# Kernel optimization log

Hardware: AMD Instinct MI355X
Metric: run time of the kernel (lower is better)

## Reference

```python
import jax, jax.numpy as jnp
import numpy as np

N = 10000
E = 320000
DIN = 256
HID = 64
HEADS = 4
LAT = 32
NEG_SLOPE = 0.2


def _layer_params(key, din, heads, out_c):
    ks = jax.random.split(key, 6)
    s_in = 1.0 / np.sqrt(din)
    return dict(
        Wl=jax.random.normal(ks[0], (din, heads * out_c), jnp.float32) * s_in,
        bl=jnp.zeros((heads * out_c,), jnp.float32),
        Wr=jax.random.normal(ks[1], (din, heads * out_c), jnp.float32) * s_in,
        br=jnp.zeros((heads * out_c,), jnp.float32),
        att=jax.random.normal(ks[2], (heads, out_c), jnp.float32) * (1.0 / np.sqrt(out_c)),
        bo=jnp.zeros((heads * out_c,), jnp.float32),
    )


def setup_inputs() -> dict:
    key = jax.random.key(0)
    ks = jax.random.split(key, 8)
    inp = {
        "x": jax.random.normal(ks[0], (N, DIN), jnp.float32),
        "edge_index": jax.random.randint(ks[1], (2, E), 0, N, jnp.int64 if jax.config.jax_enable_x64 else jnp.int32),
        "eps": jax.random.normal(ks[2], (N, LAT), jnp.float32),
    }
    p0 = _layer_params(ks[3], DIN, HEADS, HID)
    p1 = _layer_params(ks[4], HID * HEADS, HEADS, HID)
    pmu = _layer_params(ks[5], HID * HEADS, 1, LAT)
    plv = _layer_params(ks[6], HID * HEADS, 1, LAT)
    for tag, p in (("l0", p0), ("l1", p1), ("mu", pmu), ("lv", plv)):
        for k, v in p.items():
            inp[f"{k}_{tag}"] = v
    return inp


def _gatv2(h, src, dst, Wl, bl, Wr, br, att, bo, heads, out_c, concat):
    # GATv2: e_ij = att . LeakyReLU(lin_l(x_j) + lin_r(x_i)), softmax over j for each i,
    # out_i = sum_j alpha_ij * lin_l(x_j). src = j (source), dst = i (target).
    xl = (h @ Wl + bl).reshape(-1, heads, out_c)  # [N,H,C]
    xr = (h @ Wr + br).reshape(-1, heads, out_c)
    e = jax.nn.leaky_relu(xl[src] + xr[dst], NEG_SLOPE)  # [E,H,C]
    score = jnp.einsum('ehc,hc->eh', e, att)             # [E,H]
    smax = jax.ops.segment_max(score, dst, num_segments=N)
    ex = jnp.exp(score - smax[dst])
    denom = jax.ops.segment_sum(ex, dst, num_segments=N)
    alpha = ex / (denom[dst] + 1e-16)                    # [E,H]
    out = jax.ops.segment_sum(alpha[:, :, None] * xl[src], dst, num_segments=N)  # [N,H,C]
    out = out.reshape(N, heads * out_c) if concat else out.mean(axis=1)
    return out + bo


def reference(x, edge_index, eps,
              Wl_l0, bl_l0, Wr_l0, br_l0, att_l0, bo_l0,
              Wl_l1, bl_l1, Wr_l1, br_l1, att_l1, bo_l1,
              Wl_mu, bl_mu, Wr_mu, br_mu, att_mu, bo_mu,
              Wl_lv, bl_lv, Wr_lv, br_lv, att_lv, bo_lv):
    loop = jnp.arange(N, dtype=edge_index.dtype)
    src = jnp.concatenate([edge_index[0], loop])  # add self-loops (PyG default)
    dst = jnp.concatenate([edge_index[1], loop])
    h = jax.nn.elu(_gatv2(x, src, dst, Wl_l0, bl_l0, Wr_l0, br_l0, att_l0, bo_l0, HEADS, HID, True))
    h = jax.nn.elu(_gatv2(h, src, dst, Wl_l1, bl_l1, Wr_l1, br_l1, att_l1, bo_l1, HEADS, HID, True))
    mu = _gatv2(h, src, dst, Wl_mu, bl_mu, Wr_mu, br_mu, att_mu, bo_mu, 1, LAT, False)
    log_var = _gatv2(h, src, dst, Wl_lv, bl_lv, Wr_lv, br_lv, att_lv, bo_lv, 1, LAT, False)
    z = mu + eps * jnp.exp(0.5 * log_var)  # reparameterize (training mode)
    adj_recon = z @ z.T                    # [N,N] dense decode
    return (adj_recon, mu, log_var)
```

## Files before the change

kernel.cpp:

```cpp
#include <hip/hip_runtime.h>
#include <hip/hip_bf16.h>
#include <math.h>

constexpr int Nn  = 10000;
constexpr int Ed  = 320000;
constexpr int DIN = 256;
constexpr float NEG = 0.2f;

constexpr size_t OFF_XL  = 0;
constexpr size_t OFF_XR  = 2560000;
constexpr size_t OFF_H   = 5120000;
constexpr size_t OFF_XSL = 7680000;
constexpr size_t OFF_XSR = 8320000;
constexpr size_t OFF_WLC = 8960000;
constexpr size_t OFF_WRC = 8976384;
constexpr size_t OFF_BLC = 8992768;
constexpr size_t OFF_BRC = 8992832;
constexpr size_t OFF_ATT = 8992896;
constexpr size_t OFF_BOC = 8992960;
constexpr size_t OFF_INT = 9000000;
constexpr int I_DEG = 0;
constexpr int I_ROW = 16384;
constexpr int I_CUR = 32768;
constexpr int I_CSR = 49152;
static_assert(OFF_INT + (I_CSR + Ed + Nn + 4) < 100000000, "scratch fits in adj region");

__device__ __forceinline__ unsigned short f2bf(float x) {
    unsigned int u = __float_as_uint(x);
    unsigned int r = (u + 0x7FFFu + ((u >> 16) & 1u)) >> 16;
    return (unsigned short)r;
}
__device__ __forceinline__ float bf2f(unsigned short b) {
    return __uint_as_float(((unsigned int)b) << 16);
}

typedef short bf16x8 __attribute__((ext_vector_type(8)));
typedef float f32x4  __attribute__((ext_vector_type(4)));

__global__ void k_init_deg(int* deg, int n) {
    int i = blockIdx.x * blockDim.x + threadIdx.x;
    if (i < n) deg[i] = 1;
}

__global__ void k_count(const int* __restrict__ dst, int* deg, int e) {
    int i = blockIdx.x * blockDim.x + threadIdx.x;
    if (i < e) atomicAdd(&deg[dst[i]], 1);
}

__global__ void k_scan(const int* __restrict__ deg, int* row_ptr, int* cursor, int n) {
    __shared__ int sums[256];
    int t = threadIdx.x;
    int chunk = (n + 255) / 256;
    int start = t * chunk, end = min(start + chunk, n);
    int s = 0;
    for (int i = start; i < end; ++i) s += deg[i];
    sums[t] = s;
    __syncthreads();
    for (int off = 1; off < 256; off <<= 1) {
        int v = (t >= off) ? sums[t - off] : 0;
        __syncthreads();
        sums[t] += v;
        __syncthreads();
    }
    int run = sums[t] - s;
    for (int i = start; i < end; ++i) { row_ptr[i] = run; cursor[i] = run; run += deg[i]; }
    if (t == 255) row_ptr[n] = sums[255];
}

__global__ void k_scatter(const int* __restrict__ src, const int* __restrict__ dst,
                          int* cursor, int* csr, int e, int n) {
    int i = blockIdx.x * blockDim.x + threadIdx.x;
    if (i < e) {
        int d = dst[i];
        int pos = atomicAdd(&cursor[d], 1);
        csr[pos] = src[i];
    } else if (i < e + n) {
        int v = i - e;
        int pos = atomicAdd(&cursor[v], 1);
        csr[pos] = v;
    }
}

template <int NC>
__global__ __launch_bounds__(256) void k_gemm2(const float* __restrict__ A,
                                               const float* __restrict__ WL,
                                               const float* __restrict__ biasL,
                                               unsigned short* __restrict__ outL,
                                               const float* __restrict__ WR,
                                               const float* __restrict__ biasR,
                                               float* __restrict__ outR,
                                               int M) {
    constexpr int K = 256;
    __shared__ float As[32][68];
    __shared__ float WsL[32][64];
    __shared__ float WsR[32][64];
    int tid = threadIdx.x;
    int tx = tid & 15, ty = tid >> 4;
    int m0 = blockIdx.x * 64, n0 = blockIdx.y * 64;
    float accL[4][4] = {}, accR[4][4] = {};
    int am = tid >> 2, akb = (tid & 3) * 8;
    int wk = tid >> 3, wnb = (tid & 7) * 8;
    const bool arow_ok = (m0 + am) < M;
    const float* Aptr  = A  + (size_t)(m0 + am) * K + akb;
    const float* WLptr = WL + (size_t)wk * NC + n0 + wnb;
    const float* WRptr = WR + (size_t)wk * NC + n0 + wnb;

    for (int k0 = 0; k0 < K; k0 += 32) {
        float4 a0 = {0, 0, 0, 0}, a1 = {0, 0, 0, 0};
        if (arow_ok) {
            a0 = *(const float4*)(Aptr + k0);
            a1 = *(const float4*)(Aptr + k0 + 4);
        }
        float4 wl0 = *(const float4*)(WLptr + (size_t)k0 * NC);
        float4 wl1 = *(const float4*)(WLptr + (size_t)k0 * NC + 4);
        float4 wr0 = *(const float4*)(WRptr + (size_t)k0 * NC);
        float4 wr1 = *(const float4*)(WRptr + (size_t)k0 * NC + 4);
        __syncthreads();
        As[akb + 0][am] = a0.x; As[akb + 1][am] = a0.y; As[akb + 2][am] = a0.z; As[akb + 3][am] = a0.w;
        As[akb + 4][am] = a1.x; As[akb + 5][am] = a1.y; As[akb + 6][am] = a1.z; As[akb + 7][am] = a1.w;
        *(float4*)&WsL[wk][wnb]     = wl0;
        *(float4*)&WsL[wk][wnb + 4] = wl1;
        *(float4*)&WsR[wk][wnb]     = wr0;
        *(float4*)&WsR[wk][wnb + 4] = wr1;
        __syncthreads();
        #pragma unroll
        for (int k = 0; k < 32; ++k) {
            float4 a  = *(const float4*)&As[k][ty * 4];
            float4 bl = *(const float4*)&WsL[k][tx * 4];
            float4 br = *(const float4*)&WsR[k][tx * 4];
            float av[4]  = {a.x, a.y, a.z, a.w};
            float blv[4] = {bl.x, bl.y, bl.z, bl.w};
            float brv[4] = {br.x, br.y, br.z, br.w};
            #pragma unroll
            for (int i2 = 0; i2 < 4; ++i2)
                #pragma unroll
                for (int j2 = 0; j2 < 4; ++j2) {
                    accL[i2][j2] = fmaf(av[i2], blv[j2], accL[i2][j2]);
                    accR[i2][j2] = fmaf(av[i2], brv[j2], accR[i2][j2]);
                }
        }
    }
    #pragma unroll
    for (int i2 = 0; i2 < 4; ++i2) {
        int row = m0 + ty * 4 + i2;
        if (row < M) {
            int col = n0 + tx * 4;
            ushort4 s;
            s.x = f2bf(accL[i2][0] + biasL[col + 0]);
            s.y = f2bf(accL[i2][1] + biasL[col + 1]);
            s.z = f2bf(accL[i2][2] + biasL[col + 2]);
            s.w = f2bf(accL[i2][3] + biasL[col + 3]);
            *(ushort4*)&outL[(size_t)row * NC + col] = s;
            float4 o;
            o.x = accR[i2][0] + biasR[col + 0];
            o.y = accR[i2][1] + biasR[col + 1];
            o.z = accR[i2][2] + biasR[col + 2];
            o.w = accR[i2][3] + biasR[col + 3];
            *(float4*)&outR[(size_t)row * NC + col] = o;
        }
    }
}

__device__ __forceinline__ float lrelu(float x) { return x > 0.f ? x : NEG * x; }

template <bool DO_ELU>
__global__ __launch_bounds__(256) void k_gat4(const unsigned short* __restrict__ xl,
                                              const float* __restrict__ xr,
                                              const float* __restrict__ att,
                                              const float* __restrict__ bo,
                                              const int* __restrict__ row_ptr,
                                              const int* __restrict__ csr,
                                              float* __restrict__ out, int n) {
    int lane = threadIdx.x & 63;
    int node = (blockIdx.x * blockDim.x + threadIdx.x) >> 6;
    if (node >= n) return;
    int f = lane * 4;
    float4 xrr  = *(const float4*)&xr[(size_t)node * 256 + f];
    float4 attr = *(const float4*)&att[f];
    float m = -INFINITY, d = 0.f;
    float4 acc = {0.f, 0.f, 0.f, 0.f};

    int e0 = row_ptr[node], e1 = row_ptr[node + 1];
    int e = e0;
    for (; e + 1 < e1; e += 2) {
        int ja = csr[e], jb = csr[e + 1];
        ushort4 ua = *(const ushort4*)&xl[(size_t)ja * 256 + f];
        ushort4 ub = *(const ushort4*)&xl[(size_t)jb * 256 + f];
        float4 va = {bf2f(ua.x), bf2f(ua.y), bf2f(ua.z), bf2f(ua.w)};
        float4 vb = {bf2f(ub.x), bf2f(ub.y), bf2f(ub.z), bf2f(ub.w)};
        float ta = attr.x * lrelu(va.x + xrr.x) + attr.y * lrelu(va.y + xrr.y)
                 + attr.z * lrelu(va.z + xrr.z) + attr.w * lrelu(va.w + xrr.w);
        float tb = attr.x * lrelu(vb.x + xrr.x) + attr.y * lrelu(vb.y + xrr.y)
                 + attr.z * lrelu(vb.z + xrr.z) + attr.w * lrelu(vb.w + xrr.w);
        #pragma unroll
        for (int mask = 1; mask <= 8; mask <<= 1) {
            ta += __shfl_xor(ta, mask, 64);
            tb += __shfl_xor(tb, mask, 64);
        }
        float mn = fmaxf(m, fmaxf(ta, tb));
        float sc = __expf(m - mn);
        float pa = __expf(ta - mn), pb = __expf(tb - mn);
        d = d * sc + pa + pb;
        acc.x = acc.x * sc + pa * va.x + pb * vb.x;
        acc.y = acc.y * sc + pa * va.y + pb * vb.y;
        acc.z = acc.z * sc + pa * va.z + pb * vb.z;
        acc.w = acc.w * sc + pa * va.w + pb * vb.w;
        m = mn;
    }
    if (e < e1) {
        int j = csr[e];
        ushort4 u = *(const ushort4*)&xl[(size_t)j * 256 + f];
        float4 v = {bf2f(u.x), bf2f(u.y), bf2f(u.z), bf2f(u.w)};
        float t = attr.x * lrelu(v.x + xrr.x) + attr.y * lrelu(v.y + xrr.y)
                + attr.z * lrelu(v.z + xrr.z) + attr.w * lrelu(v.w + xrr.w);
        #pragma unroll
        for (int mask = 1; mask <= 8; mask <<= 1) t += __shfl_xor(t, mask, 64);
        float mn = fmaxf(m, t);
        float sc = __expf(m - mn), p = __expf(t - mn);
        d = d * sc + p;
        acc.x = acc.x * sc + p * v.x;
        acc.y = acc.y * sc + p * v.y;
        acc.z = acc.z * sc + p * v.z;
        acc.w = acc.w * sc + p * v.w;
        m = mn;
    }
    float inv = 1.f / (d + 1e-16f);
    float4 bo4 = *(const float4*)&bo[f];
    float4 o;
    o.x = acc.x * inv + bo4.x;
    o.y = acc.y * inv + bo4.y;
    o.z = acc.z * inv + bo4.z;
    o.w = acc.w * inv + bo4.w;
    if (DO_ELU) {
        o.x = o.x > 0.f ? o.x : expm1f(o.x);
        o.y = o.y > 0.f ? o.y : expm1f(o.y);
        o.z = o.z > 0.f ? o.z : expm1f(o.z);
        o.w = o.w > 0.f ? o.w : expm1f(o.w);
    }
    *(float4*)&out[(size_t)node * 256 + f] = o;
}

__global__ __launch_bounds__(256) void k_gatz(const unsigned short* __restrict__ xl,
                                              const float* __restrict__ xr,
                                              const float* __restrict__ att,
                                              const float* __restrict__ bo,
                                              const int* __restrict__ row_ptr,
                                              const int* __restrict__ csr,
                                              const float* __restrict__ eps,
                                              float* __restrict__ out0,
                                              float* __restrict__ out1,
                                              unsigned short* __restrict__ zhi,
                                              unsigned short* __restrict__ zlo, int n) {
    constexpr int C = 32;
    int lane = threadIdx.x & 63;
    int node = (blockIdx.x * blockDim.x + threadIdx.x) >> 6;
    if (node >= n) return;

    float xrr  = xr[(size_t)node * 64 + lane];
    float attr = att[lane];
    float m = -INFINITY, d = 0.f, acc = 0.f;

    int e0 = row_ptr[node], e1 = row_ptr[node + 1];
    for (int e = e0; e < e1; ++e) {
        int j = csr[e];
        float v = bf2f(xl[(size_t)j * 64 + lane]);
        float t = v + xrr;
        t = (t > 0.f) ? t : NEG * t;
        t *= attr;
        #pragma unroll
        for (int mask = C / 2; mask >= 1; mask >>= 1)
            t += __shfl_xor(t, mask, 64);
        if (t > m) {
            float sc = __expf(m - t);
            d *= sc; acc *= sc; m = t;
        }
        float p = __expf(t - m);
        d += p;
        acc = fmaf(p, v, acc);
    }
    float o = acc / (d + 1e-16f) + bo[lane];
    int c = lane & 31;
    float* op = (lane < 32) ? out0 : out1;
    op[(size_t)node * C + c] = o;
    float lvv = __shfl(o, lane + 32, 64);
    if (zhi != nullptr && lane < 32) {
        float zc = o + eps[(size_t)node * 32 + lane] * __expf(0.5f * lvv);
        unsigned short h = f2bf(zc);
        zhi[(size_t)node * 32 + lane] = h;
        zlo[(size_t)node * 32 + lane] = f2bf(zc - bf2f(h));
    }
}

__global__ void k_cat(const float* __restrict__ Wlmu, const float* __restrict__ Wllv,
                      const float* __restrict__ Wrmu, const float* __restrict__ Wrlv,
                      const float* __restrict__ blmu, const float* __restrict__ bllv,
                      const float* __restrict__ brmu, const float* __restrict__ brlv,
                      const float* __restrict__ attmu, const float* __restrict__ attlv,
                      const float* __restrict__ bomu, const float* __restrict__ bolv,
                      float* WLC, float* WRC, float* BLC, float* BRC, float* ATTC, float* BOC) {
    int i = blockIdx.x * blockDim.x + threadIdx.x;
    if (i < 256 * 64) {
        int k = i >> 6, c = i & 63;
        WLC[i] = (c < 32) ? Wlmu[k * 32 + c] : Wllv[k * 32 + c - 32];
        WRC[i] = (c < 32) ? Wrmu[k * 32 + c] : Wrlv[k * 32 + c - 32];
    }
    if (i < 64) {
        BLC[i]  = (i < 32) ? blmu[i]  : bllv[i - 32];
        BRC[i]  = (i < 32) ? brmu[i]  : brlv[i - 32];
        ATTC[i] = (i < 32) ? attmu[i] : attlv[i - 32];
        BOC[i]  = (i < 32) ? bomu[i]  : bolv[i - 32];
    }
}

constexpr int JTM = 25;

__global__ __launch_bounds__(256) void k_adjm(const unsigned short* __restrict__ zhi,
                                              const unsigned short* __restrict__ zlo,
                                              float* __restrict__ adj, int n) {
    int wave  = threadIdx.x >> 6;
    int l     = threadIdx.x & 63;
    int strip = blockIdx.y * 4 + wave;
    if (strip * 16 >= n) return;
    int i0   = strip * 16;
    int arow = i0 + (l & 15);
    int koff = (l >> 4) * 8;
    bf16x8 a_hi = *(const bf16x8*)(zhi + (size_t)arow * 32 + koff);
    bf16x8 a_lo = *(const bf16x8*)(zlo + (size_t)arow * 32 + koff);
    int crow = i0 + (l >> 4) * 4;

    for (int t = 0; t < JTM; ++t) {
        int j0   = (blockIdx.x * JTM + t) * 16;
        int brow = j0 + (l & 15);
        bf16x8 b_hi = *(const bf16x8*)(zhi + (size_t)brow * 32 + koff);
        bf16x8 b_lo = *(const bf16x8*)(zlo + (size_t)brow * 32 + koff);
        f32x4 acc = {0.f, 0.f, 0.f, 0.f};
        acc = __builtin_amdgcn_mfma_f32_16x16x32_bf16(a_hi, b_hi, acc, 0, 0, 0);
        acc = __builtin_amdgcn_mfma_f32_16x16x32_bf16(a_hi, b_lo, acc, 0, 0, 0);
        acc = __builtin_amdgcn_mfma_f32_16x16x32_bf16(a_lo, b_hi, acc, 0, 0, 0);
        size_t base = (size_t)crow * n + j0 + (l & 15);
        adj[base]                 = acc[0];
        adj[base + (size_t)n]     = acc[1];
        adj[base + (size_t)n * 2] = acc[2];
        adj[base + (size_t)n * 3] = acc[3];
    }
}

constexpr int JT = 8;
__global__ __launch_bounds__(256) void k_adj_fb(const float* __restrict__ mu,
                                                const float* __restrict__ lv,
                                                const float* __restrict__ eps,
                                                float* __restrict__ adj, int n) {
    __shared__ float Zi[32][68];
    __shared__ float Zj[32][68];
    int tid = threadIdx.x;
    int tx = tid & 15, ty = tid >> 4;
    int i0 = blockIdx.y * 64;
    int r = tid >> 2, kq = (tid & 3) * 8;

    auto load8 = [&](int row, float4& a, float4& b) {
        a = make_float4(0.f, 0.f, 0.f, 0.f);
        b = make_float4(0.f, 0.f, 0.f, 0.f);
        if (row < n) {
            float4 m0 = *(const float4*)&mu[row * 32 + kq];
            float4 l0 = *(const float4*)&lv[row * 32 + kq];
            float4 e0 = *(const float4*)&eps[row * 32 + kq];
            float4 m1 = *(const float4*)&mu[row * 32 + kq + 4];
            float4 l1 = *(const float4*)&lv[row * 32 + kq + 4];
            float4 e1 = *(const float4*)&eps[row * 32 + kq + 4];
            a.x = m0.x + e0.x * __expf(0.5f * l0.x);
            a.y = m0.y + e0.y * __expf(0.5f * l0.y);
            a.z = m0.z + e0.z * __expf(0.5f * l0.z);
            a.w = m0.w + e0.w * __expf(0.5f * l0.w);
            b.x = m1.x + e1.x * __expf(0.5f * l1.x);
            b.y = m1.y + e1.y * __expf(0.5f * l1.y);
            b.z = m1.z + e1.z * __expf(0.5f * l1.z);
            b.w = m1.w + e1.w * __expf(0.5f * l1.w);
        }
    };

    {
        float4 a, b;
        load8(i0 + r, a, b);
        Zi[kq + 0][r] = a.x; Zi[kq + 1][r] = a.y; Zi[kq + 2][r] = a.z; Zi[kq + 3][r] = a.w;
        Zi[kq + 4][r] = b.x; Zi[kq + 5][r] = b.y; Zi[kq + 6][r] = b.z; Zi[kq + 7][r] = b.w;
    }
    __syncthreads();
    float4 af[32];
    #pragma unroll
    for (int k = 0; k < 32; ++k) af[k] = *(const float4*)&Zi[k][ty * 4];

    for (int jt = 0; jt < JT; ++jt) {
        int j0 = (blockIdx.x * JT + jt) * 64;
        if (j0 >= n) break;
        {
            float4 a, b;
            load8(j0 + r, a, b);
            __syncthreads();
            Zj[kq + 0][r] = a.x; Zj[kq + 1][r] = a.y; Zj[kq + 2][r] = a.z; Zj[kq + 3][r] = a.w;
            Zj[kq + 4][r] = b.x; Zj[kq + 5][r] = b.y; Zj[kq + 6][r] = b.z; Zj[kq + 7][r] = b.w;
            __syncthreads();
        }
        float acc[4][4] = {};
        #pragma unroll
        for (int k = 0; k < 32; ++k) {
            float4 b = *(const float4*)&Zj[k][tx * 4];
            float av[4] = {af[k].x, af[k].y, af[k].z, af[k].w};
            float bv[4] = {b.x, b.y, b.z, b.w};
            #pragma unroll
            for (int i2 = 0; i2 < 4; ++i2)
                #pragma unroll
                for (int j2 = 0; j2 < 4; ++j2)
                    acc[i2][j2] = fmaf(av[i2], bv[j2], acc[i2][j2]);
        }
        int col = j0 + tx * 4;
        if (col < n) {
            #pragma unroll
            for (int i2 = 0; i2 < 4; ++i2) {
                int row = i0 + ty * 4 + i2;
                if (row < n) {
                    float4 o = {acc[i2][0], acc[i2][1], acc[i2][2], acc[i2][3]};
                    *(float4*)&adj[(size_t)row * n + col] = o;
                }
            }
        }
    }
}

extern "C" void kernel_launch(void* const* d_in, const int* in_sizes, int n_in,
                              void* d_out, int out_size, void* d_ws, size_t ws_size,
                              hipStream_t stream) {
    const float* x      = (const float*)d_in[0];
    const int*   edges  = (const int*)d_in[1];
    const float* eps    = (const float*)d_in[2];
    const float* Wl0 = (const float*)d_in[3];
    const float* bl0 = (const float*)d_in[4];
    const float* Wr0 = (const float*)d_in[5];
    const float* br0 = (const float*)d_in[6];
    const float* at0 = (const float*)d_in[7];
    const float* bo0 = (const float*)d_in[8];
    const float* Wl1 = (const float*)d_in[9];
    const float* bl1 = (const float*)d_in[10];
    const float* Wr1 = (const float*)d_in[11];
    const float* br1 = (const float*)d_in[12];
    const float* at1 = (const float*)d_in[13];
    const float* bo1 = (const float*)d_in[14];
    const float* Wlmu = (const float*)d_in[15];
    const float* blmu = (const float*)d_in[16];
    const float* Wrmu = (const float*)d_in[17];
    const float* brmu = (const float*)d_in[18];
    const float* atmu = (const float*)d_in[19];
    const float* bomu = (const float*)d_in[20];
    const float* Wllv = (const float*)d_in[21];
    const float* bllv = (const float*)d_in[22];
    const float* Wrlv = (const float*)d_in[23];
    const float* brlv = (const float*)d_in[24];
    const float* atlv = (const float*)d_in[25];
    const float* bolv = (const float*)d_in[26];

    float* base   = (float*)d_out;
    float* adj    = base;
    float* mu_out = base + (size_t)Nn * Nn;
    float* lv_out = mu_out + (size_t)Nn * 32;

    unsigned short* XLB  = (unsigned short*)(base + OFF_XL);
    float* XR  = base + OFF_XR;
    float* H   = base + OFF_H;
    unsigned short* XSLB = (unsigned short*)(base + OFF_XSL);
    float* XSR = base + OFF_XSR;
    float* WLC = base + OFF_WLC;
    float* WRC = base + OFF_WRC;
    float* BLC = base + OFF_BLC;
    float* BRC = base + OFF_BRC;
    float* ATT = base + OFF_ATT;
    float* BOC = base + OFF_BOC;
    int* ib  = (int*)(base + OFF_INT);
    int* deg = ib + I_DEG;
    int* row = ib + I_ROW;
    int* cur = ib + I_CUR;
    int* csr = ib + I_CSR;
    const int* srcp = edges;
    const int* dstp = edges + Ed;

    size_t need = (size_t)Nn * 32 * 2 * sizeof(unsigned short);
    unsigned short* zhi = (ws_size >= need) ? (unsigned short*)d_ws : nullptr;
    unsigned short* zlo = zhi ? zhi + (size_t)Nn * 32 : nullptr;

    k_init_deg<<<(Nn + 255) / 256, 256, 0, stream>>>(deg, Nn);
    k_count<<<(Ed + 255) / 256, 256, 0, stream>>>(dstp, deg, Ed);
    k_scan<<<1, 256, 0, stream>>>(deg, row, cur, Nn);
    k_scatter<<<(Ed + Nn + 255) / 256, 256, 0, stream>>>(srcp, dstp, cur, csr, Ed, Nn);

    dim3 g4(157, 4), g1(157, 1);
    k_gemm2<256><<<g4, 256, 0, stream>>>(x, Wl0, bl0, XLB, Wr0, br0, XR, Nn);
    k_gat4<true><<<2500, 256, 0, stream>>>(XLB, XR, at0, bo0, row, csr, H, Nn);
    k_gemm2<256><<<g4, 256, 0, stream>>>(H, Wl1, bl1, XLB, Wr1, br1, XR, Nn);
    k_gat4<true><<<2500, 256, 0, stream>>>(XLB, XR, at1, bo1, row, csr, H, Nn);
    k_cat<<<64, 256, 0, stream>>>(Wlmu, Wllv, Wrmu, Wrlv, blmu, bllv, brmu, brlv,
                                  atmu, atlv, bomu, bolv, WLC, WRC, BLC, BRC, ATT, BOC);
    k_gemm2<64><<<g1, 256, 0, stream>>>(H, WLC, BLC, XSLB, WRC, BRC, XSR, Nn);
    k_gatz<<<2500, 256, 0, stream>>>(XSLB, XSR, ATT, BOC, row, csr, eps,
                                     mu_out, lv_out, zhi, zlo, Nn);

    if (zhi) {
        dim3 ga(25, 157);
        k_adjm<<<ga, 256, 0, stream>>>(zhi, zlo, adj, Nn);
    } else {
        dim3 ga(20, 157);
        k_adj_fb<<<ga, 256, 0, stream>>>(mu_out, lv_out, eps, adj, Nn);
    }
}
```

Baseline: 408.5 us.

## Replace FP32 SIMT linear GEMMs with split-bf16 MFMA GEMMs and prepacked weights

Replaces the scalar FP32 shared-memory GEMM for the node linear projections with an MFMA-based kernel. Both activations and weights are split into hi/lo bf16 parts, and three MFMA products are summed to keep near-FP32 accuracy. A new one-shot kernel transposes and splits all layer weights, absorbing the old concat kernel, and k_gatz now reads the mu/logvar attention and bias vectors directly. This trades FP32 ALU throughput for matrix-core throughput. The new GEMM has no LDS reuse, so weights are re-read from global/L2 per 16-row block, and there is extra conversion work.

```diff
diff --git a/kernel.cpp b/kernel.cpp
--- a/kernel.cpp
+++ b/kernel.cpp
@@ -12,13 +12,11 @@
 constexpr size_t OFF_H   = 5120000;
 constexpr size_t OFF_XSL = 7680000;
 constexpr size_t OFF_XSR = 8320000;
-constexpr size_t OFF_WLC = 8960000;
-constexpr size_t OFF_WRC = 8976384;
-constexpr size_t OFF_BLC = 8992768;
-constexpr size_t OFF_BRC = 8992832;
-constexpr size_t OFF_ATT = 8992896;
-constexpr size_t OFF_BOC = 8992960;
-constexpr size_t OFF_INT = 9000000;
+constexpr size_t OFF_UWT = 8960000;
+constexpr size_t U0LH = 0,      U0LL = 65536,  U0RH = 131072, U0RL = 196608;
+constexpr size_t U1LH = 262144, U1LL = 327680, U1RH = 393216, U1RL = 458752;
+constexpr size_t UCLH = 524288, UCLL = 540672, UCRH = 557056, UCRL = 573440;
+constexpr size_t OFF_INT = 9300000;
 constexpr int I_DEG = 0;
 constexpr int I_ROW = 16384;
 constexpr int I_CUR = 32768;
@@ -81,82 +79,101 @@
     }
 }
 
-template <int NC>
-__global__ __launch_bounds__(256) void k_gemm2(const float* __restrict__ A,
-                                               const float* __restrict__ WL,
-                                               const float* __restrict__ biasL,
-                                               unsigned short* __restrict__ outL,
-                                               const float* __restrict__ WR,
-                                               const float* __restrict__ biasR,
-                                               float* __restrict__ outR,
-                                               int M) {
-    constexpr int K = 256;
-    __shared__ float As[32][68];
-    __shared__ float WsL[32][64];
-    __shared__ float WsR[32][64];
-    int tid = threadIdx.x;
-    int tx = tid & 15, ty = tid >> 4;
-    int m0 = blockIdx.x * 64, n0 = blockIdx.y * 64;
-    float accL[4][4] = {}, accR[4][4] = {};
-    int am = tid >> 2, akb = (tid & 3) * 8;
-    int wk = tid >> 3, wnb = (tid & 7) * 8;
-    const bool arow_ok = (m0 + am) < M;
-    const float* Aptr  = A  + (size_t)(m0 + am) * K + akb;
-    const float* WLptr = WL + (size_t)wk * NC + n0 + wnb;
-    const float* WRptr = WR + (size_t)wk * NC + n0 + wnb;
-
-    for (int k0 = 0; k0 < K; k0 += 32) {
-        float4 a0 = {0, 0, 0, 0}, a1 = {0, 0, 0, 0};
-        if (arow_ok) {
-            a0 = *(const float4*)(Aptr + k0);
-            a1 = *(const float4*)(Aptr + k0 + 4);
-        }
-        float4 wl0 = *(const float4*)(WLptr + (size_t)k0 * NC);
-        float4 wl1 = *(const float4*)(WLptr + (size_t)k0 * NC + 4);
-        float4 wr0 = *(const float4*)(WRptr + (size_t)k0 * NC);
-        float4 wr1 = *(const float4*)(WRptr + (size_t)k0 * NC + 4);
-        __syncthreads();
-        As[akb + 0][am] = a0.x; As[akb + 1][am] = a0.y; As[akb + 2][am] = a0.z; As[akb + 3][am] = a0.w;
-        As[akb + 4][am] = a1.x; As[akb + 5][am] = a1.y; As[akb + 6][am] = a1.z; As[akb + 7][am] = a1.w;
-        *(float4*)&WsL[wk][wnb]     = wl0;
-        *(float4*)&WsL[wk][wnb + 4] = wl1;
-        *(float4*)&WsR[wk][wnb]     = wr0;
-        *(float4*)&WsR[wk][wnb + 4] = wr1;
-        __syncthreads();
+__global__ void k_wt_all(const float* __restrict__ Wl0, const float* __restrict__ Wr0,
+                         const float* __restrict__ Wl1, const float* __restrict__ Wr1,
+                         const float* __restrict__ Wlmu, const float* __restrict__ Wllv,
+                         const float* __restrict__ Wrmu, const float* __restrict__ Wrlv,
+                         unsigned short* __restrict__ wt) {
+    int i = blockIdx.x * blockDim.x + threadIdx.x;
+    if (i >= 262144 + 32768) return;
+    float v;
+    size_t hioff, idx;
+    int losz;
+    if (i < 262144) {
+        int widx = i >> 16, rem = i & 65535;
+        int c = rem >> 8, k = rem & 255;
+        const float* W = (widx == 0) ? Wl0 : (widx == 1) ? Wr0 : (widx == 2) ? Wl1 : Wr1;
+        v = W[k * 256 + c];
+        hioff = (size_t)widx * 131072;
+        idx = rem; losz = 65536;
+    } else {
+        int rem2 = i - 262144;
+        int matC = rem2 >> 14, r3 = rem2 & 16383;
+        int c = r3 >> 8, k = r3 & 255;
+        if (matC == 0) v = (c < 32) ? Wlmu[k * 32 + c] : Wllv[k * 32 + c - 32];
+        else           v = (c < 32) ? Wrmu[k * 32 + c] : Wrlv[k * 32 + c - 32];
+        hioff = UCLH + (size_t)matC * 32768;
+        idx = r3; losz = 16384;
+    }
+    unsigned short h = f2bf(v);
+    wt[hioff + idx]        = h;
+    wt[hioff + losz + idx] = f2bf(v - bf2f(h));
+}
+
+template <int NC, bool SPLITB>
+__global__ __launch_bounds__(256) void k_gemm2m(
+        const float* __restrict__ A,
+        const unsigned short* __restrict__ wLh, const unsigned short* __restrict__ wLl,
+        const unsigned short* __restrict__ wRh, const unsigned short* __restrict__ wRl,
+        const float* __restrict__ bLa, const float* __restrict__ bLb,
+        const float* __restrict__ bRa, const float* __restrict__ bRb,
+        unsigned short* __restrict__ outL, float* __restrict__ outR, int M) {
+    constexpr int JT_N  = NC / 16;
+    constexpr int TILES = 2 * JT_N;
+    constexpr int TPW   = TILES / 4;
+    int w = threadIdx.x >> 6;
+    int l = threadIdx.x & 63;
+    int i0 = blockIdx.x * 16;
+    if (i0 >= M) return;
+    int arow  = i0 + (l & 15);
+    int kbase = (l >> 4) * 8;
+    bf16x8 a_hi[8], a_lo[8];
+    #pragma unroll
+    for (int c = 0; c < 8; ++c) {
+        float4 f0 = *(const float4*)(A + (size_t)arow * 256 + c * 32 + kbase);
+        float4 f1 = *(const float4*)(A + (size_t)arow * 256 + c * 32 + kbase + 4);
+        float fv[8] = {f0.x, f0.y, f0.z, f0.w, f1.x, f1.y, f1.z, f1.w};
+        bf16x8 h, lo;
         #pragma unroll
-        for (int k = 0; k < 32; ++k) {
-            float4 a  = *(const float4*)&As[k][ty * 4];
-            float4 bl = *(const float4*)&WsL[k][tx * 4];
-            float4 br = *(const float4*)&WsR[k][tx * 4];
-            float av[4]  = {a.x, a.y, a.z, a.w};
-            float blv[4] = {bl.x, bl.y, bl.z, bl.w};
-            float brv[4] = {br.x, br.y, br.z, br.w};
+        for (int q = 0; q < 8; ++q) {
+            unsigned short hh = f2bf(fv[q]);
+            h[q]  = (short)hh;
+            lo[q] = (short)f2bf(fv[q] - bf2f(hh));
+        }
+        a_hi[c] = h;
+        a_lo[c] = lo;
+    }
+    int crow = i0 + (l >> 4) * 4;
+    int ncol = l & 15;
+
+    #pragma unroll
+    for (int t = 0; t < TPW; ++t) {
+        int jt  = w * TPW + t;
+        int mat = jt / JT_N;
+        int j0  = (jt % JT_N) * 16;
+        int col = j0 + ncol;
+        const unsigned short* bh_p = ((mat == 0) ? wLh : wRh) + (size_t)col * 256 + kbase;
+        const unsigned short* bl_p = ((mat == 0) ? wLl : wRl) + (size_t)col * 256 + kbase;
+        f32x4 acc = {0.f, 0.f, 0.f, 0.f};
+        #pragma unroll
+        for (int c = 0; c < 8; ++c) {
+            bf16x8 bh = *(const bf16x8*)(bh_p + c * 32);
+            bf16x8 bl = *(const bf16x8*)(bl_p + c * 32);
+            acc = __builtin_amdgcn_mfma_f32_16x16x32_bf16(a_hi[c], bh, acc, 0, 0, 0);
+            acc = __builtin_amdgcn_mfma_f32_16x16x32_bf16(a_hi[c], bl, acc, 0, 0, 0);
+            acc = __builtin_amdgcn_mfma_f32_16x16x32_bf16(a_lo[c], bh, acc, 0, 0, 0);
+        }
+        float bias;
+        if (mat == 0) bias = (!SPLITB || col < 32) ? bLa[col] : bLb[col - 32];
+        else          bias = (!SPLITB || col < 32) ? bRa[col] : bRb[col - 32];
+        if (mat == 0) {
             #pragma unroll
-            for (int i2 = 0; i2 < 4; ++i2)
-                #pragma unroll
-                for (int j2 = 0; j2 < 4; ++j2) {
-                    accL[i2][j2] = fmaf(av[i2], blv[j2], accL[i2][j2]);
-                    accR[i2][j2] = fmaf(av[i2], brv[j2], accR[i2][j2]);
-                }
-        }
-    }
-    #pragma unroll
-    for (int i2 = 0; i2 < 4; ++i2) {
-        int row = m0 + ty * 4 + i2;
-        if (row < M) {
-            int col = n0 + tx * 4;
-            ushort4 s;
-            s.x = f2bf(accL[i2][0] + biasL[col + 0]);
-            s.y = f2bf(accL[i2][1] + biasL[col + 1]);
-            s.z = f2bf(accL[i2][2] + biasL[col + 2]);
-            s.w = f2bf(accL[i2][3] + biasL[col + 3]);
-            *(ushort4*)&outL[(size_t)row * NC + col] = s;
-            float4 o;
-            o.x = accR[i2][0] + biasR[col + 0];
-            o.y = accR[i2][1] + biasR[col + 1];
-            o.z = accR[i2][2] + biasR[col + 2];
-            o.w = accR[i2][3] + biasR[col + 3];
-            *(float4*)&outR[(size_t)row * NC + col] = o;
+            for (int r = 0; r < 4; ++r)
+                outL[(size_t)(crow + r) * NC + col] = f2bf(acc[r] + bias);
+        } else {
+            #pragma unroll
+            for (int r = 0; r < 4; ++r)
+                outR[(size_t)(crow + r) * NC + col] = acc[r] + bias;
         }
     }
 }
@@ -242,8 +259,10 @@
 
 __global__ __launch_bounds__(256) void k_gatz(const unsigned short* __restrict__ xl,
                                               const float* __restrict__ xr,
-                                              const float* __restrict__ att,
-                                              const float* __restrict__ bo,
+                                              const float* __restrict__ atmu,
+                                              const float* __restrict__ atlv,
+                                              const float* __restrict__ bomu,
+                                              const float* __restrict__ bolv,
                                               const int* __restrict__ row_ptr,
                                               const int* __restrict__ csr,
                                               const float* __restrict__ eps,
@@ -257,7 +276,7 @@
     if (node >= n) return;
 
     float xrr  = xr[(size_t)node * 64 + lane];
-    float attr = att[lane];
+    float attr = (lane < 32) ? atmu[lane] : atlv[lane - 32];
     float m = -INFINITY, d = 0.f, acc = 0.f;
 
     int e0 = row_ptr[node], e1 = row_ptr[node + 1];
@@ -278,7 +297,8 @@
         d += p;
         acc = fmaf(p, v, acc);
     }
-    float o = acc / (d + 1e-16f) + bo[lane];
+    float bov = (lane < 32) ? bomu[lane] : bolv[lane - 32];
+    float o = acc / (d + 1e-16f) + bov;
     int c = lane & 31;
     float* op = (lane < 32) ? out0 : out1;
     op[(size_t)node * C + c] = o;
@@ -288,27 +308,6 @@
         unsigned short h = f2bf(zc);
         zhi[(size_t)node * 32 + lane] = h;
         zlo[(size_t)node * 32 + lane] = f2bf(zc - bf2f(h));
-    }
-}
-
-__global__ void k_cat(const float* __restrict__ Wlmu, const float* __restrict__ Wllv,
-                      const float* __restrict__ Wrmu, const float* __restrict__ Wrlv,
-                      const float* __restrict__ blmu, const float* __restrict__ bllv,
-                      const float* __restrict__ brmu, const float* __restrict__ brlv,
-                      const float* __restrict__ attmu, const float* __restrict__ attlv,
-                      const float* __restrict__ bomu, const float* __restrict__ bolv,
-                      float* WLC, float* WRC, float* BLC, float* BRC, float* ATTC, float* BOC) {
-    int i = blockIdx.x * blockDim.x + threadIdx.x;
-    if (i < 256 * 64) {
-        int k = i >> 6, c = i & 63;
-        WLC[i] = (c < 32) ? Wlmu[k * 32 + c] : Wllv[k * 32 + c - 32];
-        WRC[i] = (c < 32) ? Wrmu[k * 32 + c] : Wrlv[k * 32 + c - 32];
-    }
-    if (i < 64) {
-        BLC[i]  = (i < 32) ? blmu[i]  : bllv[i - 32];
-        BRC[i]  = (i < 32) ? brmu[i]  : brlv[i - 32];
-        ATTC[i] = (i < 32) ? attmu[i] : attlv[i - 32];
-        BOC[i]  = (i < 32) ? bomu[i]  : bolv[i - 32];
     }
 }
 
@@ -467,12 +466,7 @@
     float* H   = base + OFF_H;
     unsigned short* XSLB = (unsigned short*)(base + OFF_XSL);
     float* XSR = base + OFF_XSR;
-    float* WLC = base + OFF_WLC;
-    float* WRC = base + OFF_WRC;
-    float* BLC = base + OFF_BLC;
-    float* BRC = base + OFF_BRC;
-    float* ATT = base + OFF_ATT;
-    float* BOC = base + OFF_BOC;
+    unsigned short* uwt = (unsigned short*)(base + OFF_UWT);
     int* ib  = (int*)(base + OFF_INT);
     int* deg = ib + I_DEG;
     int* row = ib + I_ROW;
@@ -490,15 +484,21 @@
     k_scan<<<1, 256, 0, stream>>>(deg, row, cur, Nn);
     k_scatter<<<(Ed + Nn + 255) / 256, 256, 0, stream>>>(srcp, dstp, cur, csr, Ed, Nn);
 
-    dim3 g4(157, 4), g1(157, 1);
-    k_gemm2<256><<<g4, 256, 0, stream>>>(x, Wl0, bl0, XLB, Wr0, br0, XR, Nn);
+    k_wt_all<<<(262144 + 32768 + 255) / 256, 256, 0, stream>>>(
+        Wl0, Wr0, Wl1, Wr1, Wlmu, Wllv, Wrmu, Wrlv, uwt);
+
+    k_gemm2m<256, false><<<625, 256, 0, stream>>>(
+        x, uwt + U0LH, uwt + U0LL, uwt + U0RH, uwt + U0RL,
+        bl0, bl0, br0, br0, XLB, XR, Nn);
     k_gat4<true><<<2500, 256, 0, stream>>>(XLB, XR, at0, bo0, row, csr, H, Nn);
-    k_gemm2<256><<<g4, 256, 0, stream>>>(H, Wl1, bl1, XLB, Wr1, br1, XR, Nn);
+    k_gemm2m<256, false><<<625, 256, 0, stream>>>(
+        H, uwt + U1LH, uwt + U1LL, uwt + U1RH, uwt + U1RL,
+        bl1, bl1, br1, br1, XLB, XR, Nn);
     k_gat4<true><<<2500, 256, 0, stream>>>(XLB, XR, at1, bo1, row, csr, H, Nn);
-    k_cat<<<64, 256, 0, stream>>>(Wlmu, Wllv, Wrmu, Wrlv, blmu, bllv, brmu, brlv,
-                                  atmu, atlv, bomu, bolv, WLC, WRC, BLC, BRC, ATT, BOC);
-    k_gemm2<64><<<g1, 256, 0, stream>>>(H, WLC, BLC, XSLB, WRC, BRC, XSR, Nn);
-    k_gatz<<<2500, 256, 0, stream>>>(XSLB, XSR, ATT, BOC, row, csr, eps,
+    k_gemm2m<64, true><<<625, 256, 0, stream>>>(
+        H, uwt + UCLH, uwt + UCLL, uwt + UCRH, uwt + UCRL,
+        blmu, bllv, brmu, brlv, XSLB, XSR, Nn);
+    k_gatz<<<2500, 256, 0, stream>>>(XSLB, XSR, atmu, atlv, bomu, bolv, row, csr, eps,
                                      mu_out, lv_out, zhi, zlo, Nn);
 
     if (zhi) {
```

New measurement: 432.2 us. 5.8% more time.
